# Performance work log

Hardware: AMD Instinct MI355X
Metric: run time of the kernel (lower is better)

## Reference

```python
import jax, jax.numpy as jnp
import numpy as np

TAU = 0.5          # proto_tau
TOPK = 3           # slot_topk
BETA = 0.5         # soft-topk temperature
BETA_SUP = 0.4     # support_beta
T_SUP = 1.6        # support_tsup
KAPPA_FEAT = 1.0   # support_kappa_feat
CMAX = 64          # num classes


def setup_inputs() -> dict:
    key = jax.random.key(0)
    k0, k1, k2, k3 = jax.random.split(key, 4)
    B, M, D, K = 128, 64, 512, 4096
    feats_bmd = jax.random.normal(k0, (B, M, D), jnp.float32)
    slot_prob = jax.random.uniform(k1, (B, M), jnp.float32)
    slot_mask = jnp.ones((M,), jnp.float32)
    S_slots = jax.random.normal(k2, (B, M, D), jnp.float32)
    C = jax.random.normal(k3, (K, D), jnp.float32)
    # every class gets K//CMAX prototypes (torch.unique loop covers all classes)
    C_cls = jnp.arange(K, dtype=jnp.int32) % CMAX
    alpha = jnp.array(1.0, jnp.float32)
    return dict(feats_bmd=feats_bmd, slot_prob=slot_prob, slot_mask=slot_mask,
                S_slots=S_slots, C=C, C_cls=C_cls, alpha=alpha)


def _l2norm(x, eps=1e-12):
    return x / jnp.maximum(jnp.linalg.norm(x, axis=-1, keepdims=True), eps)


def _soft_topk_weights(p, mask, k=TOPK, beta=BETA):
    # p: (B,M), mask: (1,M)
    p = p * mask
    _, topi = jax.lax.top_k(p, k)                          # (B,k)
    keep = jnp.zeros_like(p).at[jnp.arange(p.shape[0])[:, None], topi].set(1.0)
    q = p * keep
    z = (q - q.mean(axis=1, keepdims=True)) / beta
    w = jax.nn.softmax(z, axis=1) * mask
    return w / jnp.maximum(w.sum(axis=1, keepdims=True), 1e-8)


def _class_lse(sim, cls, num_classes, tau=TAU):
    # segmented logsumexp over prototypes grouped by class id (replaces the
    # per-class masked_fill loop in the original).
    B, M, K = sim.shape
    s = sim.reshape(B * M, K).T                                   # (K, BM)
    xmax = jax.ops.segment_max(s, cls, num_segments=num_classes)  # (C, BM)
    e = jnp.exp((s - xmax[cls]) / tau)
    ssum = jax.ops.segment_sum(e, cls, num_segments=num_classes)  # (C, BM)
    evi = xmax + tau * jnp.log(jnp.maximum(ssum, 1e-8))
    return evi.T.reshape(B, M, num_classes)


def _top1_plus_support(evi, P, S_slots):
    # evi: (B,M,C), P: (B,M), S_slots: (B,M,D)
    B, M, C = evi.shape
    score = evi * P[:, :, None]
    top1_idx = jnp.argmax(score, axis=1)                    # (B,C)
    top1_val = jnp.max(score, axis=1)                       # (B,C)
    P_sup = jax.nn.softmax(jnp.log(P + 1e-8) / T_SUP, axis=1)  # (B,M)
    S = _l2norm(S_slots)
    top1_feat = jnp.take_along_axis(S, top1_idx[:, :, None], axis=1)  # (B,C,D)
    cos = jnp.maximum(jnp.einsum('bmd,bcd->bmc', S, top1_feat), 0.0)
    w_red = KAPPA_FEAT * cos
    support_raw = evi + jnp.log(jnp.maximum(P_sup, 1e-8))[:, :, None] - w_red
    is_top1 = jnp.arange(M)[None, :, None] == top1_idx[:, None, :]    # (B,M,C)
    support_raw = jnp.where(is_top1, -10000.0, support_raw)
    support_val = jax.nn.logsumexp(support_raw, axis=1)
    return top1_val + BETA_SUP * support_val


def reference(feats_bmd, slot_prob, slot_mask, S_slots, C, C_cls, alpha):
    w = _soft_topk_weights(slot_prob, slot_mask[None, :])
    f = _l2norm(feats_bmd)
    sim = jnp.einsum('bmd,kd->bmk', f, C)        # (B,M,K) similarity GEMM
    evi_all = _class_lse(sim, C_cls, CMAX)       # (B,M,Cmax)
    proto_logits = _top1_plus_support(evi_all, w, S_slots)
    return alpha * proto_logits                  # (B, Cmax)
```

## Files before the change

### kernel.cpp

```cpp
#include <hip/hip_runtime.h>
#include <stdint.h>


typedef short   short8_t  __attribute__((ext_vector_type(8)));
typedef unsigned short ushort8_t __attribute__((ext_vector_type(8)));
typedef float   floatx4   __attribute__((ext_vector_type(4)));

#define B_N   128
#define M_N   64
#define D_N   512
#define K_N   4096
#define ROWS  8192

__device__ __forceinline__ unsigned short f2bf(float f){
  unsigned u = __float_as_uint(f);
  u = (u + 0x7FFFu + ((u >> 16) & 1u)) >> 16;
  return (unsigned short)u;
}
__device__ __forceinline__ float bf2f(unsigned short s){
  return __uint_as_float(((unsigned)s) << 16);
}

__global__ __launch_bounds__(256) void k_prep(
    const float* __restrict__ feats, const float* __restrict__ Cm,
    unsigned short* __restrict__ fhi, unsigned short* __restrict__ flo,
    unsigned short* __restrict__ chi, unsigned short* __restrict__ clo){
  const int bid = blockIdx.x;
  const bool isF = bid < 2048;
  const int lane = threadIdx.x & 63;
  const int row  = (isF ? bid : bid - 2048) * 4 + (threadIdx.x >> 6);
  const float* src = isF ? feats : Cm;
  const float4* r = (const float4*)(src + (size_t)row * D_N);
  float4 a = r[lane*2], c = r[lane*2 + 1];
  float inv = 1.f;
  if(isF){
    float ss = a.x*a.x + a.y*a.y + a.z*a.z + a.w*a.w
             + c.x*c.x + c.y*c.y + c.z*c.z + c.w*c.w;
    #pragma unroll
    for(int off = 32; off > 0; off >>= 1) ss += __shfl_xor(ss, off);
    inv = 1.f / fmaxf(sqrtf(ss), 1e-12f);
  }
  float v[8] = {a.x*inv, a.y*inv, a.z*inv, a.w*inv, c.x*inv, c.y*inv, c.z*inv, c.w*inv};
  ushort8_t h, L;
  #pragma unroll
  for(int i = 0; i < 8; ++i){
    h[i] = f2bf(v[i]);
    L[i] = f2bf(v[i] - bf2f(h[i]));
  }
  unsigned short* hi = isF ? fhi : chi;
  unsigned short* lo = isF ? flo : clo;
  ((ushort8_t*)(hi + (size_t)row * D_N))[lane] = h;
  ((ushort8_t*)(lo + (size_t)row * D_N))[lane] = L;
}

__device__ __forceinline__ floatx4 mfma16(short8_t a, short8_t b, floatx4 c){
  return __builtin_amdgcn_mfma_f32_16x16x32_bf16(a, b, c, 0, 0, 0);
}

__global__ __launch_bounds__(512, 2) void k_gemm_lse(
    const unsigned short* __restrict__ fhi, const unsigned short* __restrict__ flo,
    const unsigned short* __restrict__ chi, const unsigned short* __restrict__ clo,
    float* __restrict__ part){
  __shared__ char smem[98304];
  const int bid = blockIdx.x;
  const int pg  = bid & 7;
  const int rg  = bid >> 3;
  const int tid = threadIdx.x;
  const int w = tid >> 6, lane = tid & 63;
  const int wr = w >> 2, wc = w & 3;
  const int l15 = lane & 15, l4 = lane >> 4;

  const int arow = tid >> 2, aslot = tid & 3;
  const char* aH = (const char*)fhi + ((size_t)(rg*128 + arow))*1024 + aslot*16;
  const char* aL = (const char*)flo + ((size_t)(rg*128 + arow))*1024 + aslot*16;
  const char* bH = (const char*)chi + ((size_t)(pg*512 + arow))*1024 + aslot*16;
  const char* bL = (const char*)clo + ((size_t)(pg*512 + arow))*1024 + aslot*16;
  const int ldst = tid * 16;

  const int fro = l15*64 + l4*16;
  const int aBase = wr*4096;
  const int bBase = 16384 + wc*4096;

  floatx4 sim[4][4];
  float  cacc[4][4][4];
  #pragma unroll
  for(int rf = 0; rf < 4; ++rf)
    #pragma unroll
    for(int cf = 0; cf < 4; ++cf){
      sim[rf][cf] = (floatx4){0.f,0.f,0.f,0.f};
      #pragma unroll
      for(int e = 0; e < 4; ++e) cacc[rf][cf][e] = 0.f;
    }

  short8_t p0, p1, p2, p3, p4, p5;
  p0 = *(const short8_t*)(aH);
  p1 = *(const short8_t*)(aL);
  p2 = *(const short8_t*)(bH);
  p3 = *(const short8_t*)(bH + 131072);
  p4 = *(const short8_t*)(bL);
  p5 = *(const short8_t*)(bL + 131072);
  {
    char* buf = smem;
    *(short8_t*)(buf + ldst)                 = p0;
    *(short8_t*)(buf + 8192  + ldst)         = p1;
    *(short8_t*)(buf + 16384 + ldst)         = p2;
    *(short8_t*)(buf + 16384 + 8192 + ldst)  = p3;
    *(short8_t*)(buf + 32768 + ldst)         = p4;
    *(short8_t*)(buf + 32768 + 8192 + ldst)  = p5;
  }

  #pragma unroll 1
  for(int s = 0; s < 32; ++s){
    if(s < 31){
      const int sn = s + 1;
      const int da = (sn & 15) * 64;
      const size_t db = (size_t)(sn >> 4) * 262144 + da;
      p0 = *(const short8_t*)(aH + da);
      p1 = *(const short8_t*)(aL + da);
      p2 = *(const short8_t*)(bH + db);
      p3 = *(const short8_t*)(bH + 131072 + db);
      p4 = *(const short8_t*)(bL + db);
      p5 = *(const short8_t*)(bL + 131072 + db);
    }

    __syncthreads();
    char* buf = smem + (s & 1) * 49152;

    __builtin_amdgcn_s_setprio(1);
    short8_t ah[4], al[4];
    #pragma unroll
    for(int rf = 0; rf < 4; ++rf){
      ah[rf] = *(const short8_t*)(buf + aBase + rf*1024 + fro);
      al[rf] = *(const short8_t*)(buf + 8192 + aBase + rf*1024 + fro);
    }
    #pragma unroll
    for(int cf = 0; cf < 4; ++cf){
      short8_t bh = *(const short8_t*)(buf + bBase + cf*1024 + fro);
      short8_t bl = *(const short8_t*)(buf + 16384 + bBase + cf*1024 + fro);
      #pragma unroll
      for(int rf = 0; rf < 4; ++rf){
        sim[rf][cf] = mfma16(ah[rf], bh, sim[rf][cf]);
        sim[rf][cf] = mfma16(al[rf], bh, sim[rf][cf]);
        sim[rf][cf] = mfma16(ah[rf], bl, sim[rf][cf]);
      }
    }
    __builtin_amdgcn_s_setprio(0);

    if(s < 31){
      char* nb = smem + ((s + 1) & 1) * 49152;
      *(short8_t*)(nb + ldst)                 = p0;
      *(short8_t*)(nb + 8192  + ldst)         = p1;
      *(short8_t*)(nb + 16384 + ldst)         = p2;
      *(short8_t*)(nb + 16384 + 8192 + ldst)  = p3;
      *(short8_t*)(nb + 32768 + ldst)         = p4;
      *(short8_t*)(nb + 32768 + 8192 + ldst)  = p5;
    }

    if((s & 15) == 15){
      #pragma unroll
      for(int rf = 0; rf < 4; ++rf)
        #pragma unroll
        for(int cf = 0; cf < 4; ++cf){
          #pragma unroll
          for(int e = 0; e < 4; ++e)
            cacc[rf][cf][e] += __expf(2.0f * sim[rf][cf][e]);
          sim[rf][cf] = (floatx4){0.f,0.f,0.f,0.f};
        }
    }
  }

  __syncthreads();
  if(wc > 0){
    float* sl = (float*)(smem + (wr*3 + wc - 1) * 16384);
    #pragma unroll
    for(int rf = 0; rf < 4; ++rf)
      #pragma unroll
      for(int cf = 0; cf < 4; ++cf)
        #pragma unroll
        for(int e = 0; e < 4; ++e)
          sl[(rf*16 + l4*4 + e)*64 + cf*16 + l15] = cacc[rf][cf][e];
  }
  __syncthreads();
  if(wc == 0){
    const float* s0 = (const float*)(smem + (wr*3 + 0) * 16384);
    const float* s1 = (const float*)(smem + (wr*3 + 1) * 16384);
    const float* s2 = (const float*)(smem + (wr*3 + 2) * 16384);
    #pragma unroll
    for(int rf = 0; rf < 4; ++rf)
      #pragma unroll
      for(int cf = 0; cf < 4; ++cf)
        #pragma unroll
        for(int e = 0; e < 4; ++e){
          const int idx = (rf*16 + l4*4 + e)*64 + cf*16 + l15;
          const float v = cacc[rf][cf][e] + s0[idx] + s1[idx] + s2[idx];
          const int row = rg*128 + wr*64 + rf*16 + l4*4 + e;
          part[((size_t)pg*ROWS + row)*64 + cf*16 + l15] = v;
        }
  }
}

#define SPAD 516
__global__ __launch_bounds__(256) void k_epi(
    const float* __restrict__ part, const float* __restrict__ S_raw,
    const float* __restrict__ prob, const float* __restrict__ maskp,
    const float* __restrict__ alpha_p, float* __restrict__ out){
  __shared__ float Ss[64 * SPAD];
  __shared__ float evi[64 * 64];
  __shared__ float w_s[64], lps_s[64], t1v[64];
  __shared__ int   t1i[64];
  __shared__ float red[16 * 64];
  const int b = blockIdx.x, tid = threadIdx.x;

  if(tid < 64){
    const int m = tid;
    const float mk = maskp[m];
    float p = prob[b*M_N + m] * mk;
    float pw = p, keep = 0.f;
    for(int it = 0; it < 3; ++it){
      float v = pw; int idx = m;
      #pragma unroll
      for(int off = 32; off > 0; off >>= 1){
        float ov = __shfl_xor(v, off);
        int   oi = __shfl_xor(idx, off);
        if(ov > v || (ov == v && oi < idx)){ v = ov; idx = oi; }
      }
      if(m == idx){ keep = 1.f; pw = -1e30f; }
    }
    float q = p * keep;
    float s = q;
    #pragma unroll
    for(int off = 32; off > 0; off >>= 1) s += __shfl_xor(s, off);
    float z = (q - s * (1.f/64.f)) * 2.0f;
    float zm = z;
    #pragma unroll
    for(int off = 32; off > 0; off >>= 1) zm = fmaxf(zm, __shfl_xor(zm, off));
    float e = expf(z - zm);
    float es = e;
    #pragma unroll
    for(int off = 32; off > 0; off >>= 1) es += __shfl_xor(es, off);
    float wv = (e / es) * mk;
    float ws = wv;
    #pragma unroll
    for(int off = 32; off > 0; off >>= 1) ws += __shfl_xor(ws, off);
    wv = wv / fmaxf(ws, 1e-8f);
    w_s[m] = wv;
    float l = logf(wv + 1e-8f) * (1.0f/1.6f);
    float lm = l;
    #pragma unroll
    for(int off = 32; off > 0; off >>= 1) lm = fmaxf(lm, __shfl_xor(lm, off));
    float ee = expf(l - lm);
    float ees = ee;
    #pragma unroll
    for(int off = 32; off > 0; off >>= 1) ees += __shfl_xor(ees, off);
    lps_s[m] = logf(fmaxf(ee / ees, 1e-8f));
  }

  for(int i = tid; i < 4096; i += 256){
    float s = 0.f;
    #pragma unroll
    for(int pg = 0; pg < 8; ++pg)
      s += part[(size_t)pg*ROWS*64 + (size_t)b*4096 + i];
    evi[i] = 0.5f * logf(s);
  }
  const float4* sg = (const float4*)(S_raw + (size_t)b * 32768);
  for(int i = tid; i < 8192; i += 256){
    int r = i >> 7, c4 = i & 127;
    *(float4*)&Ss[r*SPAD + c4*4] = sg[i];
  }
  __syncthreads();

  {
    const int lane = tid & 63;
    for(int it = 0; it < 16; ++it){
      const int row = it*4 + (tid >> 6);
      float4 x = *(const float4*)&Ss[row*SPAD + lane*8];
      float4 y = *(const float4*)&Ss[row*SPAD + lane*8 + 4];
      float ss = x.x*x.x + x.y*x.y + x.z*x.z + x.w*x.w
               + y.x*y.x + y.y*y.y + y.z*y.z + y.w*y.w;
      #pragma unroll
      for(int off = 32; off > 0; off >>= 1) ss += __shfl_xor(ss, off);
      float inv = 1.f / fmaxf(sqrtf(ss), 1e-12f);
      x.x*=inv; x.y*=inv; x.z*=inv; x.w*=inv;
      y.x*=inv; y.y*=inv; y.z*=inv; y.w*=inv;
      *(float4*)&Ss[row*SPAD + lane*8]     = x;
      *(float4*)&Ss[row*SPAD + lane*8 + 4] = y;
    }
  }
  __syncthreads();

  if(tid < 64){
    float bv = -1e30f; int bi = 0;
    for(int m = 0; m < 64; ++m){
      float sc = evi[m*64 + tid] * w_s[m];
      if(sc > bv){ bv = sc; bi = m; }
    }
    t1v[tid] = bv; t1i[tid] = bi;
  }
  __syncthreads();

  const int mi = tid >> 4, ci = tid & 15;
  float acc[4][4];
  #pragma unroll
  for(int i = 0; i < 4; ++i)
    #pragma unroll
    for(int j = 0; j < 4; ++j) acc[i][j] = 0.f;
  int tr[4];
  #pragma unroll
  for(int q = 0; q < 4; ++q) tr[q] = t1i[ci*4 + q];

  for(int d4 = 0; d4 < 128; ++d4){
    float4 sv[4], tv[4];
    #pragma unroll
    for(int q = 0; q < 4; ++q) sv[q] = *(const float4*)&Ss[(mi*4 + q)*SPAD + d4*4];
    #pragma unroll
    for(int q = 0; q < 4; ++q) tv[q] = *(const float4*)&Ss[tr[q]*SPAD + d4*4];
    #pragma unroll
    for(int i = 0; i < 4; ++i)
      #pragma unroll
      for(int j = 0; j < 4; ++j)
        acc[i][j] += sv[i].x*tv[j].x + sv[i].y*tv[j].y + sv[i].z*tv[j].z + sv[i].w*tv[j].w;
  }

  float ps[4] = {0.f, 0.f, 0.f, 0.f};
  #pragma unroll
  for(int i = 0; i < 4; ++i){
    const int m = mi*4 + i;
    #pragma unroll
    for(int q = 0; q < 4; ++q){
      const int c = ci*4 + q;
      float sr = evi[m*64 + c] + lps_s[m] - fmaxf(acc[i][q], 0.f);
      ps[q] += (m == tr[q]) ? 0.f : expf(sr);
    }
  }
  #pragma unroll
  for(int q = 0; q < 4; ++q) red[mi*64 + ci*4 + q] = ps[q];
  __syncthreads();

  if(tid < 64){
    float s = 0.f;
    for(int i = 0; i < 16; ++i) s += red[i*64 + tid];
    out[b*64 + tid] = alpha_p[0] * (t1v[tid] + 0.4f * logf(s));
  }
}

extern "C" void kernel_launch(void* const* d_in, const int* in_sizes, int n_in,
                              void* d_out, int out_size, void* d_ws, size_t ws_size,
                              hipStream_t stream){
  const float* feats     = (const float*)d_in[0];
  const float* slot_prob = (const float*)d_in[1];
  const float* slot_mask = (const float*)d_in[2];
  const float* S_slots   = (const float*)d_in[3];
  const float* Cmat      = (const float*)d_in[4];
  const float* alpha     = (const float*)d_in[6];

  char* ws = (char*)d_ws;
  unsigned short* fhi = (unsigned short*)(ws);
  unsigned short* flo = (unsigned short*)(ws + (8  << 20));
  unsigned short* chi = (unsigned short*)(ws + (16 << 20));
  unsigned short* clo = (unsigned short*)(ws + (20 << 20));
  float* part  = (float*)(ws + (24 << 20));
  float* outp  = (float*)d_out;

  k_prep<<<dim3(3072), dim3(256), 0, stream>>>(feats, Cmat, fhi, flo, chi, clo);
  k_gemm_lse<<<dim3(512), dim3(512), 0, stream>>>(fhi, flo, chi, clo, part);
  k_epi<<<dim3(128), dim3(256), 0, stream>>>(part, S_slots, slot_prob, slot_mask,
                                             alpha, outp);
}
```

Measured before the change: 230.7 us.

## Halve GEMM column tile, pad LDS rows, and swizzle block order for L2 reuse

The GEMM+LSE kernel now uses a 128x256 tile instead of 128x512, with 64 K-steps over smaller LDS buffers. Rows are padded to 80 bytes to cut bank conflicts, and the launch bound now asks for 4 blocks per CU. Block indices are remapped so that neighbouring blocks share prototype column groups, aiming for better L2 reuse. The prep kernel switches to coalesced float4/ushort4 accesses. The trade-off is fewer MFMAs per LDS load, twice as many barriers, and possible register pressure under the higher occupancy target.

```diff
diff --git a/kernel.cpp b/kernel.cpp
--- a/kernel.cpp
+++ b/kernel.cpp
@@ -3,7 +3,6 @@
 
 
 typedef short   short8_t  __attribute__((ext_vector_type(8)));
-typedef unsigned short ushort8_t __attribute__((ext_vector_type(8)));
 typedef float   floatx4   __attribute__((ext_vector_type(4)));
 
 #define B_N   128
@@ -31,7 +30,8 @@
   const int row  = (isF ? bid : bid - 2048) * 4 + (threadIdx.x >> 6);
   const float* src = isF ? feats : Cm;
   const float4* r = (const float4*)(src + (size_t)row * D_N);
-  float4 a = r[lane*2], c = r[lane*2 + 1];
+  float4 a = r[lane];
+  float4 c = r[lane + 64];
   float inv = 1.f;
   if(isF){
     float ss = a.x*a.x + a.y*a.y + a.z*a.z + a.w*a.w
@@ -40,127 +40,123 @@
     for(int off = 32; off > 0; off >>= 1) ss += __shfl_xor(ss, off);
     inv = 1.f / fmaxf(sqrtf(ss), 1e-12f);
   }
-  float v[8] = {a.x*inv, a.y*inv, a.z*inv, a.w*inv, c.x*inv, c.y*inv, c.z*inv, c.w*inv};
-  ushort8_t h, L;
-  #pragma unroll
-  for(int i = 0; i < 8; ++i){
-    h[i] = f2bf(v[i]);
-    L[i] = f2bf(v[i] - bf2f(h[i]));
+  float va[4] = {a.x*inv, a.y*inv, a.z*inv, a.w*inv};
+  float vc[4] = {c.x*inv, c.y*inv, c.z*inv, c.w*inv};
+  ushort4 ha, hc, la, lc;
+  unsigned short* pa = (unsigned short*)&ha; unsigned short* pc = (unsigned short*)&hc;
+  unsigned short* qa = (unsigned short*)&la; unsigned short* qc = (unsigned short*)&lc;
+  #pragma unroll
+  for(int i = 0; i < 4; ++i){
+    pa[i] = f2bf(va[i]); qa[i] = f2bf(va[i] - bf2f(pa[i]));
+    pc[i] = f2bf(vc[i]); qc[i] = f2bf(vc[i] - bf2f(pc[i]));
   }
   unsigned short* hi = isF ? fhi : chi;
   unsigned short* lo = isF ? flo : clo;
-  ((ushort8_t*)(hi + (size_t)row * D_N))[lane] = h;
-  ((ushort8_t*)(lo + (size_t)row * D_N))[lane] = L;
+  ushort4* ho = (ushort4*)(hi + (size_t)row * D_N);
+  ushort4* loo = (ushort4*)(lo + (size_t)row * D_N);
+  ho[lane] = ha;  ho[lane + 64] = hc;
+  loo[lane] = la; loo[lane + 64] = lc;
 }
 
 __device__ __forceinline__ floatx4 mfma16(short8_t a, short8_t b, floatx4 c){
   return __builtin_amdgcn_mfma_f32_16x16x32_bf16(a, b, c, 0, 0, 0);
 }
 
-__global__ __launch_bounds__(512, 2) void k_gemm_lse(
+__global__ __launch_bounds__(512, 4) void k_gemm_lse(
     const unsigned short* __restrict__ fhi, const unsigned short* __restrict__ flo,
     const unsigned short* __restrict__ chi, const unsigned short* __restrict__ clo,
     float* __restrict__ part){
-  __shared__ char smem[98304];
+  __shared__ char smem[81920];
   const int bid = blockIdx.x;
-  const int pg  = bid & 7;
-  const int rg  = bid >> 3;
+  const int p  = bid & 7;
+  const int x  = bid >> 3;
+  const int rg = p*8 + (x & 7);
+  const int pg = x >> 3;
   const int tid = threadIdx.x;
   const int w = tid >> 6, lane = tid & 63;
   const int wr = w >> 2, wc = w & 3;
   const int l15 = lane & 15, l4 = lane >> 4;
 
-  const int arow = tid >> 2, aslot = tid & 3;
-  const char* aH = (const char*)fhi + ((size_t)(rg*128 + arow))*1024 + aslot*16;
-  const char* aL = (const char*)flo + ((size_t)(rg*128 + arow))*1024 + aslot*16;
-  const char* bH = (const char*)chi + ((size_t)(pg*512 + arow))*1024 + aslot*16;
-  const char* bL = (const char*)clo + ((size_t)(pg*512 + arow))*1024 + aslot*16;
-  const int ldst = tid * 16;
-
-  const int fro = l15*64 + l4*16;
-  const int aBase = wr*4096;
-  const int bBase = 16384 + wc*4096;
-
-  floatx4 sim[4][4];
-  float  cacc[4][4][4];
+  const int srow = tid >> 2, ss = tid & 3;
+  const int woff = srow*80 + ss*16;
+  const char* aH = (const char*)fhi + ((size_t)(rg*128 + srow))*1024 + ss*16;
+  const char* aL = (const char*)flo + ((size_t)(rg*128 + srow))*1024 + ss*16;
+  const char* bH = (const char*)chi + ((size_t)(pg*512 + srow))*1024 + ss*16;
+  const char* bL = (const char*)clo + ((size_t)(pg*512 + srow))*1024 + ss*16;
+
+  const int fro = l15*80 + l4*16;
+  const int aR = wr*5120;
+  const int bR = 20480 + wc*2560;
+
+  floatx4 sim[4][2];
+  float   cacc[4][2][4];
   #pragma unroll
   for(int rf = 0; rf < 4; ++rf)
     #pragma unroll
-    for(int cf = 0; cf < 4; ++cf){
+    for(int cf = 0; cf < 2; ++cf){
       sim[rf][cf] = (floatx4){0.f,0.f,0.f,0.f};
       #pragma unroll
       for(int e = 0; e < 4; ++e) cacc[rf][cf][e] = 0.f;
     }
 
-  short8_t p0, p1, p2, p3, p4, p5;
+  short8_t p0, p1, p2, p3;
   p0 = *(const short8_t*)(aH);
   p1 = *(const short8_t*)(aL);
   p2 = *(const short8_t*)(bH);
-  p3 = *(const short8_t*)(bH + 131072);
-  p4 = *(const short8_t*)(bL);
-  p5 = *(const short8_t*)(bL + 131072);
-  {
-    char* buf = smem;
-    *(short8_t*)(buf + ldst)                 = p0;
-    *(short8_t*)(buf + 8192  + ldst)         = p1;
-    *(short8_t*)(buf + 16384 + ldst)         = p2;
-    *(short8_t*)(buf + 16384 + 8192 + ldst)  = p3;
-    *(short8_t*)(buf + 32768 + ldst)         = p4;
-    *(short8_t*)(buf + 32768 + 8192 + ldst)  = p5;
-  }
+  p3 = *(const short8_t*)(bL);
+  *(short8_t*)(smem + woff)         = p0;
+  *(short8_t*)(smem + 10240 + woff) = p1;
+  *(short8_t*)(smem + 20480 + woff) = p2;
+  *(short8_t*)(smem + 30720 + woff) = p3;
 
   #pragma unroll 1
-  for(int s = 0; s < 32; ++s){
-    if(s < 31){
+  for(int s = 0; s < 64; ++s){
+    if(s < 63){
       const int sn = s + 1;
       const int da = (sn & 15) * 64;
-      const size_t db = (size_t)(sn >> 4) * 262144 + da;
+      const size_t db = (size_t)(sn >> 4) * 131072 + da;
       p0 = *(const short8_t*)(aH + da);
       p1 = *(const short8_t*)(aL + da);
       p2 = *(const short8_t*)(bH + db);
-      p3 = *(const short8_t*)(bH + 131072 + db);
-      p4 = *(const short8_t*)(bL + db);
-      p5 = *(const short8_t*)(bL + 131072 + db);
+      p3 = *(const short8_t*)(bL + db);
     }
 
     __syncthreads();
-    char* buf = smem + (s & 1) * 49152;
+    const char* buf = smem + (s & 1) * 40960;
 
     __builtin_amdgcn_s_setprio(1);
-    short8_t ah[4], al[4];
+    short8_t bh[2], bl[2];
+    #pragma unroll
+    for(int cf = 0; cf < 2; ++cf){
+      bh[cf] = *(const short8_t*)(buf + bR + cf*1280 + fro);
+      bl[cf] = *(const short8_t*)(buf + 10240 + bR + cf*1280 + fro);
+    }
     #pragma unroll
     for(int rf = 0; rf < 4; ++rf){
-      ah[rf] = *(const short8_t*)(buf + aBase + rf*1024 + fro);
-      al[rf] = *(const short8_t*)(buf + 8192 + aBase + rf*1024 + fro);
-    }
-    #pragma unroll
-    for(int cf = 0; cf < 4; ++cf){
-      short8_t bh = *(const short8_t*)(buf + bBase + cf*1024 + fro);
-      short8_t bl = *(const short8_t*)(buf + 16384 + bBase + cf*1024 + fro);
-      #pragma unroll
-      for(int rf = 0; rf < 4; ++rf){
-        sim[rf][cf] = mfma16(ah[rf], bh, sim[rf][cf]);
-        sim[rf][cf] = mfma16(al[rf], bh, sim[rf][cf]);
-        sim[rf][cf] = mfma16(ah[rf], bl, sim[rf][cf]);
+      short8_t ah = *(const short8_t*)(buf + aR + rf*1280 + fro);
+      short8_t al = *(const short8_t*)(buf + 10240 + aR + rf*1280 + fro);
+      #pragma unroll
+      for(int cf = 0; cf < 2; ++cf){
+        sim[rf][cf] = mfma16(ah, bh[cf], sim[rf][cf]);
+        sim[rf][cf] = mfma16(al, bh[cf], sim[rf][cf]);
+        sim[rf][cf] = mfma16(ah, bl[cf], sim[rf][cf]);
       }
     }
     __builtin_amdgcn_s_setprio(0);
 
-    if(s < 31){
-      char* nb = smem + ((s + 1) & 1) * 49152;
-      *(short8_t*)(nb + ldst)                 = p0;
-      *(short8_t*)(nb + 8192  + ldst)         = p1;
-      *(short8_t*)(nb + 16384 + ldst)         = p2;
-      *(short8_t*)(nb + 16384 + 8192 + ldst)  = p3;
-      *(short8_t*)(nb + 32768 + ldst)         = p4;
-      *(short8_t*)(nb + 32768 + 8192 + ldst)  = p5;
+    if(s < 63){
+      char* nb = smem + ((s + 1) & 1) * 40960;
+      *(short8_t*)(nb + woff)         = p0;
+      *(short8_t*)(nb + 10240 + woff) = p1;
+      *(short8_t*)(nb + 20480 + woff) = p2;
+      *(short8_t*)(nb + 30720 + woff) = p3;
     }
 
     if((s & 15) == 15){
       #pragma unroll
       for(int rf = 0; rf < 4; ++rf)
         #pragma unroll
-        for(int cf = 0; cf < 4; ++cf){
+        for(int cf = 0; cf < 2; ++cf){
           #pragma unroll
           for(int e = 0; e < 4; ++e)
             cacc[rf][cf][e] += __expf(2.0f * sim[rf][cf][e]);
@@ -170,31 +166,29 @@
   }
 
   __syncthreads();
-  if(wc > 0){
-    float* sl = (float*)(smem + (wr*3 + wc - 1) * 16384);
+  const int pairId = wc & 1;
+  float* sl = (float*)smem + (wr*2 + pairId) * 2176;
+  if(wc >= 2){
     #pragma unroll
     for(int rf = 0; rf < 4; ++rf)
       #pragma unroll
-      for(int cf = 0; cf < 4; ++cf)
+      for(int cf = 0; cf < 2; ++cf)
         #pragma unroll
         for(int e = 0; e < 4; ++e)
-          sl[(rf*16 + l4*4 + e)*64 + cf*16 + l15] = cacc[rf][cf][e];
-  }
-  __syncthreads();
-  if(wc == 0){
-    const float* s0 = (const float*)(smem + (wr*3 + 0) * 16384);
-    const float* s1 = (const float*)(smem + (wr*3 + 1) * 16384);
-    const float* s2 = (const float*)(smem + (wr*3 + 2) * 16384);
+          sl[(rf*16 + l4*4 + e)*33 + cf*16 + l15] = cacc[rf][cf][e];
+  }
+  __syncthreads();
+  if(wc < 2){
     #pragma unroll
     for(int rf = 0; rf < 4; ++rf)
       #pragma unroll
-      for(int cf = 0; cf < 4; ++cf)
+      for(int cf = 0; cf < 2; ++cf)
         #pragma unroll
         for(int e = 0; e < 4; ++e){
-          const int idx = (rf*16 + l4*4 + e)*64 + cf*16 + l15;
-          const float v = cacc[rf][cf][e] + s0[idx] + s1[idx] + s2[idx];
+          const float v = cacc[rf][cf][e] + sl[(rf*16 + l4*4 + e)*33 + cf*16 + l15];
           const int row = rg*128 + wr*64 + rf*16 + l4*4 + e;
-          part[((size_t)pg*ROWS + row)*64 + cf*16 + l15] = v;
+          const int cls = wc*32 + cf*16 + l15;
+          part[((size_t)pg*ROWS + row)*64 + cls] = v;
         }
   }
 }
```

Result: no change. 230.0 us (-0.3%).

## Swizzle GEMM LDS tiles, remap block grouping, pad epilogue shared arrays

Applied to the files above, without the earlier changes.

The GEMM kernel now writes and reads its LDS tiles through an XOR swizzle on the 16-byte slot index, aimed at removing bank conflicts on the MFMA fragment reads. It also remaps block IDs so consecutive blocks share the same prototype group, for better L2 reuse, and it hoists the B fragments into registers instead of the A fragments. The prep kernel uses coalesced float4 strides, and the epilogue pads the evi and reduction arrays and interleaves rows across threads to reduce LDS bank conflicts. Holding more fragments in registers may add register pressure.

```diff
diff --git a/kernel.cpp b/kernel.cpp
--- a/kernel.cpp
+++ b/kernel.cpp
@@ -3,7 +3,6 @@
 
 
 typedef short   short8_t  __attribute__((ext_vector_type(8)));
-typedef unsigned short ushort8_t __attribute__((ext_vector_type(8)));
 typedef float   floatx4   __attribute__((ext_vector_type(4)));
 
 #define B_N   128
@@ -31,7 +30,8 @@
   const int row  = (isF ? bid : bid - 2048) * 4 + (threadIdx.x >> 6);
   const float* src = isF ? feats : Cm;
   const float4* r = (const float4*)(src + (size_t)row * D_N);
-  float4 a = r[lane*2], c = r[lane*2 + 1];
+  float4 a = r[lane];
+  float4 c = r[lane + 64];
   float inv = 1.f;
   if(isF){
     float ss = a.x*a.x + a.y*a.y + a.z*a.z + a.w*a.w
@@ -40,17 +40,22 @@
     for(int off = 32; off > 0; off >>= 1) ss += __shfl_xor(ss, off);
     inv = 1.f / fmaxf(sqrtf(ss), 1e-12f);
   }
-  float v[8] = {a.x*inv, a.y*inv, a.z*inv, a.w*inv, c.x*inv, c.y*inv, c.z*inv, c.w*inv};
-  ushort8_t h, L;
-  #pragma unroll
-  for(int i = 0; i < 8; ++i){
-    h[i] = f2bf(v[i]);
-    L[i] = f2bf(v[i] - bf2f(h[i]));
+  float va[4] = {a.x*inv, a.y*inv, a.z*inv, a.w*inv};
+  float vc[4] = {c.x*inv, c.y*inv, c.z*inv, c.w*inv};
+  ushort4 ha, hc, la, lc;
+  unsigned short* pa = (unsigned short*)&ha; unsigned short* pc = (unsigned short*)&hc;
+  unsigned short* qa = (unsigned short*)&la; unsigned short* qc = (unsigned short*)&lc;
+  #pragma unroll
+  for(int i = 0; i < 4; ++i){
+    pa[i] = f2bf(va[i]); qa[i] = f2bf(va[i] - bf2f(pa[i]));
+    pc[i] = f2bf(vc[i]); qc[i] = f2bf(vc[i] - bf2f(pc[i]));
   }
   unsigned short* hi = isF ? fhi : chi;
   unsigned short* lo = isF ? flo : clo;
-  ((ushort8_t*)(hi + (size_t)row * D_N))[lane] = h;
-  ((ushort8_t*)(lo + (size_t)row * D_N))[lane] = L;
+  ushort4* ho  = (ushort4*)(hi + (size_t)row * D_N);
+  ushort4* loo = (ushort4*)(lo + (size_t)row * D_N);
+  ho[lane] = ha;  ho[lane + 64] = hc;
+  loo[lane] = la; loo[lane + 64] = lc;
 }
 
 __device__ __forceinline__ floatx4 mfma16(short8_t a, short8_t b, floatx4 c){
@@ -63,26 +68,28 @@
     float* __restrict__ part){
   __shared__ char smem[98304];
   const int bid = blockIdx.x;
-  const int pg  = bid & 7;
-  const int rg  = bid >> 3;
+  const int p  = bid & 7;
+  const int x  = bid >> 3;
+  const int rg = p*8 + (x & 7);
+  const int pg = x >> 3;
   const int tid = threadIdx.x;
   const int w = tid >> 6, lane = tid & 63;
   const int wr = w >> 2, wc = w & 3;
   const int l15 = lane & 15, l4 = lane >> 4;
 
-  const int arow = tid >> 2, aslot = tid & 3;
-  const char* aH = (const char*)fhi + ((size_t)(rg*128 + arow))*1024 + aslot*16;
-  const char* aL = (const char*)flo + ((size_t)(rg*128 + arow))*1024 + aslot*16;
-  const char* bH = (const char*)chi + ((size_t)(pg*512 + arow))*1024 + aslot*16;
-  const char* bL = (const char*)clo + ((size_t)(pg*512 + arow))*1024 + aslot*16;
-  const int ldst = tid * 16;
-
-  const int fro = l15*64 + l4*16;
-  const int aBase = wr*4096;
-  const int bBase = 16384 + wc*4096;
+  const int srow = tid >> 2, ss = tid & 3;
+  const int woff = srow*64 + ((ss ^ ((srow >> 1) & 3)) << 4);
+  const char* aH = (const char*)fhi + ((size_t)(rg*128 + srow))*1024 + ss*16;
+  const char* aL = (const char*)flo + ((size_t)(rg*128 + srow))*1024 + ss*16;
+  const char* bH = (const char*)chi + ((size_t)(pg*512 + srow))*1024 + ss*16;
+  const char* bL = (const char*)clo + ((size_t)(pg*512 + srow))*1024 + ss*16;
+
+  const int fro = l15*64 + ((l4 ^ ((l15 >> 1) & 3)) << 4);
+  const int aR = wr*4096;
+  const int bR = 16384 + wc*4096;
 
   floatx4 sim[4][4];
-  float  cacc[4][4][4];
+  float   cacc[4][4][4];
   #pragma unroll
   for(int rf = 0; rf < 4; ++rf)
     #pragma unroll
@@ -99,15 +106,12 @@
   p3 = *(const short8_t*)(bH + 131072);
   p4 = *(const short8_t*)(bL);
   p5 = *(const short8_t*)(bL + 131072);
-  {
-    char* buf = smem;
-    *(short8_t*)(buf + ldst)                 = p0;
-    *(short8_t*)(buf + 8192  + ldst)         = p1;
-    *(short8_t*)(buf + 16384 + ldst)         = p2;
-    *(short8_t*)(buf + 16384 + 8192 + ldst)  = p3;
-    *(short8_t*)(buf + 32768 + ldst)         = p4;
-    *(short8_t*)(buf + 32768 + 8192 + ldst)  = p5;
-  }
+  *(short8_t*)(smem + woff)                = p0;
+  *(short8_t*)(smem + 8192  + woff)        = p1;
+  *(short8_t*)(smem + 16384 + woff)        = p2;
+  *(short8_t*)(smem + 16384 + 8192 + woff) = p3;
+  *(short8_t*)(smem + 32768 + woff)        = p4;
+  *(short8_t*)(smem + 32768 + 8192 + woff) = p5;
 
   #pragma unroll 1
   for(int s = 0; s < 32; ++s){
@@ -124,36 +128,36 @@
     }
 
     __syncthreads();
-    char* buf = smem + (s & 1) * 49152;
+    const char* buf = smem + (s & 1) * 49152;
 
     __builtin_amdgcn_s_setprio(1);
-    short8_t ah[4], al[4];
+    short8_t bh[4], bl[4];
+    #pragma unroll
+    for(int cf = 0; cf < 4; ++cf){
+      bh[cf] = *(const short8_t*)(buf + bR + cf*1024 + fro);
+      bl[cf] = *(const short8_t*)(buf + 16384 + bR + cf*1024 + fro);
+    }
     #pragma unroll
     for(int rf = 0; rf < 4; ++rf){
-      ah[rf] = *(const short8_t*)(buf + aBase + rf*1024 + fro);
-      al[rf] = *(const short8_t*)(buf + 8192 + aBase + rf*1024 + fro);
-    }
-    #pragma unroll
-    for(int cf = 0; cf < 4; ++cf){
-      short8_t bh = *(const short8_t*)(buf + bBase + cf*1024 + fro);
-      short8_t bl = *(const short8_t*)(buf + 16384 + bBase + cf*1024 + fro);
-      #pragma unroll
-      for(int rf = 0; rf < 4; ++rf){
-        sim[rf][cf] = mfma16(ah[rf], bh, sim[rf][cf]);
-        sim[rf][cf] = mfma16(al[rf], bh, sim[rf][cf]);
-        sim[rf][cf] = mfma16(ah[rf], bl, sim[rf][cf]);
+      short8_t ah = *(const short8_t*)(buf + aR + rf*1024 + fro);
+      short8_t al = *(const short8_t*)(buf + 8192 + aR + rf*1024 + fro);
+      #pragma unroll
+      for(int cf = 0; cf < 4; ++cf){
+        sim[rf][cf] = mfma16(ah, bh[cf], sim[rf][cf]);
+        sim[rf][cf] = mfma16(al, bh[cf], sim[rf][cf]);
+        sim[rf][cf] = mfma16(ah, bl[cf], sim[rf][cf]);
       }
     }
     __builtin_amdgcn_s_setprio(0);
 
     if(s < 31){
       char* nb = smem + ((s + 1) & 1) * 49152;
-      *(short8_t*)(nb + ldst)                 = p0;
-      *(short8_t*)(nb + 8192  + ldst)         = p1;
-      *(short8_t*)(nb + 16384 + ldst)         = p2;
-      *(short8_t*)(nb + 16384 + 8192 + ldst)  = p3;
-      *(short8_t*)(nb + 32768 + ldst)         = p4;
-      *(short8_t*)(nb + 32768 + 8192 + ldst)  = p5;
+      *(short8_t*)(nb + woff)                = p0;
+      *(short8_t*)(nb + 8192  + woff)        = p1;
+      *(short8_t*)(nb + 16384 + woff)        = p2;
+      *(short8_t*)(nb + 16384 + 8192 + woff) = p3;
+      *(short8_t*)(nb + 32768 + woff)        = p4;
+      *(short8_t*)(nb + 32768 + 8192 + woff) = p5;
     }
 
     if((s & 15) == 15){
@@ -205,10 +209,10 @@
     const float* __restrict__ prob, const float* __restrict__ maskp,
     const float* __restrict__ alpha_p, float* __restrict__ out){
   __shared__ float Ss[64 * SPAD];
-  __shared__ float evi[64 * 64];
+  __shared__ float evi[64 * 65];
   __shared__ float w_s[64], lps_s[64], t1v[64];
   __shared__ int   t1i[64];
-  __shared__ float red[16 * 64];
+  __shared__ float red[64 * 17];
   const int b = blockIdx.x, tid = threadIdx.x;
 
   if(tid < 64){
@@ -260,7 +264,7 @@
     #pragma unroll
     for(int pg = 0; pg < 8; ++pg)
       s += part[(size_t)pg*ROWS*64 + (size_t)b*4096 + i];
-    evi[i] = 0.5f * logf(s);
+    evi[(i >> 6)*65 + (i & 63)] = 0.5f * logf(s);
   }
   const float4* sg = (const float4*)(S_raw + (size_t)b * 32768);
   for(int i = tid; i < 8192; i += 256){
@@ -273,17 +277,17 @@
     const int lane = tid & 63;
     for(int it = 0; it < 16; ++it){
       const int row = it*4 + (tid >> 6);
-      float4 x = *(const float4*)&Ss[row*SPAD + lane*8];
-      float4 y = *(const float4*)&Ss[row*SPAD + lane*8 + 4];
-      float ss = x.x*x.x + x.y*x.y + x.z*x.z + x.w*x.w
-               + y.x*y.x + y.y*y.y + y.z*y.z + y.w*y.w;
-      #pragma unroll
-      for(int off = 32; off > 0; off >>= 1) ss += __shfl_xor(ss, off);
-      float inv = 1.f / fmaxf(sqrtf(ss), 1e-12f);
-      x.x*=inv; x.y*=inv; x.z*=inv; x.w*=inv;
-      y.x*=inv; y.y*=inv; y.z*=inv; y.w*=inv;
-      *(float4*)&Ss[row*SPAD + lane*8]     = x;
-      *(float4*)&Ss[row*SPAD + lane*8 + 4] = y;
+      float4 xv = *(const float4*)&Ss[row*SPAD + lane*8];
+      float4 yv = *(const float4*)&Ss[row*SPAD + lane*8 + 4];
+      float ssq = xv.x*xv.x + xv.y*xv.y + xv.z*xv.z + xv.w*xv.w
+                + yv.x*yv.x + yv.y*yv.y + yv.z*yv.z + yv.w*yv.w;
+      #pragma unroll
+      for(int off = 32; off > 0; off >>= 1) ssq += __shfl_xor(ssq, off);
+      float inv = 1.f / fmaxf(sqrtf(ssq), 1e-12f);
+      xv.x*=inv; xv.y*=inv; xv.z*=inv; xv.w*=inv;
+      yv.x*=inv; yv.y*=inv; yv.z*=inv; yv.w*=inv;
+      *(float4*)&Ss[row*SPAD + lane*8]     = xv;
+      *(float4*)&Ss[row*SPAD + lane*8 + 4] = yv;
     }
   }
   __syncthreads();
@@ -291,14 +295,14 @@
   if(tid < 64){
     float bv = -1e30f; int bi = 0;
     for(int m = 0; m < 64; ++m){
-      float sc = evi[m*64 + tid] * w_s[m];
+      float sc = evi[m*65 + tid] * w_s[m];
       if(sc > bv){ bv = sc; bi = m; }
     }
     t1v[tid] = bv; t1i[tid] = bi;
   }
   __syncthreads();
 
-  const int mi = tid >> 4, ci = tid & 15;
+  const int mi = tid & 15, ci = tid >> 4;
   float acc[4][4];
   #pragma unroll
   for(int i = 0; i < 4; ++i)
@@ -311,34 +315,34 @@
   for(int d4 = 0; d4 < 128; ++d4){
     float4 sv[4], tv[4];
     #pragma unroll
-    for(int q = 0; q < 4; ++q) sv[q] = *(const float4*)&Ss[(mi*4 + q)*SPAD + d4*4];
-    #pragma unroll
     for(int q = 0; q < 4; ++q) tv[q] = *(const float4*)&Ss[tr[q]*SPAD + d4*4];
     #pragma unroll
+    for(int i = 0; i < 4; ++i) sv[i] = *(const float4*)&Ss[(mi + 16*i)*SPAD + d4*4];
+    #pragma unroll
     for(int i = 0; i < 4; ++i)
       #pragma unroll
-      for(int j = 0; j < 4; ++j)
-        acc[i][j] += sv[i].x*tv[j].x + sv[i].y*tv[j].y + sv[i].z*tv[j].z + sv[i].w*tv[j].w;
+      for(int q = 0; q < 4; ++q)
+        acc[i][q] += sv[i].x*tv[q].x + sv[i].y*tv[q].y + sv[i].z*tv[q].z + sv[i].w*tv[q].w;
   }
 
   float ps[4] = {0.f, 0.f, 0.f, 0.f};
   #pragma unroll
   for(int i = 0; i < 4; ++i){
-    const int m = mi*4 + i;
+    const int m = mi + 16*i;
     #pragma unroll
     for(int q = 0; q < 4; ++q){
       const int c = ci*4 + q;
-      float sr = evi[m*64 + c] + lps_s[m] - fmaxf(acc[i][q], 0.f);
+      float sr = evi[m*65 + c] + lps_s[m] - fmaxf(acc[i][q], 0.f);
       ps[q] += (m == tr[q]) ? 0.f : expf(sr);
     }
   }
   #pragma unroll
-  for(int q = 0; q < 4; ++q) red[mi*64 + ci*4 + q] = ps[q];
+  for(int q = 0; q < 4; ++q) red[(ci*4 + q)*17 + mi] = ps[q];
   __syncthreads();
 
   if(tid < 64){
     float s = 0.f;
-    for(int i = 0; i < 16; ++i) s += red[i*64 + tid];
+    for(int i = 0; i < 16; ++i) s += red[tid*17 + i];
     out[b*64 + tid] = alpha_p[0] * (t1v[tid] + 0.4f * logf(s));
   }
 }
```

Result: faster. 225.3 us (-2.4%).
